# Optimization experiments

Measured on AMD Instinct MI355X. Metric: run time of the kernel, lower is better.

Reference implementation:

```python
import jax, jax.numpy as jnp
import numpy as np

B, D, E, T, H = 16384, 1024, 8, 4, 512


def setup_inputs() -> dict:
    key = jax.random.key(0)
    ks = jax.random.split(key, 7)
    s_e = 1.0 / np.sqrt(D)
    s_t = 1.0 / np.sqrt(H)
    return {
        "x": jax.random.normal(ks[0], (B, D), dtype=jnp.float32),
        "We": jax.random.uniform(ks[1], (E, D, H), minval=-s_e, maxval=s_e, dtype=jnp.float32),
        "be": jax.random.uniform(ks[2], (E, H), minval=-s_e, maxval=s_e, dtype=jnp.float32),
        "Wg": jax.random.uniform(ks[3], (T, D, E), minval=-s_e, maxval=s_e, dtype=jnp.float32),
        "bg": jax.random.uniform(ks[4], (T, E), minval=-s_e, maxval=s_e, dtype=jnp.float32),
        "Wt": jax.random.uniform(ks[5], (T, H, 1), minval=-s_t, maxval=s_t, dtype=jnp.float32),
        "bt": jax.random.uniform(ks[6], (T, 1), minval=-s_t, maxval=s_t, dtype=jnp.float32),
    }


def reference(x, We, be, Wg, bg, Wt, bt):
    # Experts: [B, E, H] -- batched GEMM over all experts at once
    expert_out = jnp.einsum("bd,edh->beh", x, We) + be[None, :, :]
    # Gates per task: logits [B, T, E], softmax over experts
    gate_logits = jnp.einsum("bd,tde->bte", x, Wg) + bg[None, :, :]
    gate_w = jax.nn.softmax(gate_logits, axis=-1)
    # Weighted sum of expert outputs per task: [B, T, H]
    mixed = jnp.einsum("bte,beh->bth", gate_w, expert_out)
    # Task heads: [B, T, 1]
    task_out = jnp.einsum("bth,tho->bto", mixed, Wt) + bt[None, :, :]
    # Match original: list of T tensors [B, 1] -> stacked [T, B, 1]
    return jnp.transpose(task_out, (1, 0, 2))
```

## Files before the change

### kernel.cpp

```cpp
#include <hip/hip_runtime.h>
#include <math.h>


typedef float  f32x4  __attribute__((ext_vector_type(4)));
typedef short  bf16x8 __attribute__((ext_vector_type(8)));

#define WFRAG_OFF_BYTES 262272
#define SCHED_FENCE() __builtin_amdgcn_sched_barrier(0)

__device__ __forceinline__ void cvt_pair(float f0, float f1, unsigned int& hi, unsigned int& lo) {
  unsigned int u0 = __float_as_uint(f0), u1 = __float_as_uint(f1);
  unsigned int r0 = u0 + 0x7FFFu + ((u0 >> 16) & 1u);
  unsigned int r1 = u1 + 0x7FFFu + ((u1 >> 16) & 1u);
  float h0 = __uint_as_float(r0 & 0xFFFF0000u);
  float h1 = __uint_as_float(r1 & 0xFFFF0000u);
  hi = (r0 >> 16) | (r1 & 0xFFFF0000u);
  float l0 = f0 - h0, l1 = f1 - h1;
  unsigned int s0 = __float_as_uint(l0), s1 = __float_as_uint(l1);
  unsigned int q0 = s0 + 0x7FFFu + ((s0 >> 16) & 1u);
  unsigned int q1 = s1 + 0x7FFFu + ((s1 >> 16) & 1u);
  lo = (q0 >> 16) | (q1 & 0xFFFF0000u);
}

__device__ __forceinline__ unsigned int cvtpk_bf16(float a, float b) {
  unsigned int r;
  asm("v_cvt_pk_bf16_f32 %0, %1, %2" : "=v"(r) : "v"(a), "v"(b));
  return r;
}
__device__ __forceinline__ void cvt_pair_fast(float f0, float f1, unsigned int& hi, unsigned int& lo) {
  unsigned int h = cvtpk_bf16(f0, f1);
  float h0 = __uint_as_float(h << 16);
  float h1 = __uint_as_float(h & 0xFFFF0000u);
  lo = cvtpk_bf16(f0 - h0, f1 - h1);
  hi = h;
}

__global__ __launch_bounds__(256) void mmoe_precompute(
    const float* __restrict__ We, const float* __restrict__ be,
    const float* __restrict__ Wg, const float* __restrict__ Wt,
    float* __restrict__ ws)
{
  float* Wcomb = ws;
  float* cbias = ws + 65536;
  const int tid = threadIdx.x, lane = tid & 63, w = tid >> 6;
  const int pairid = blockIdx.x * 4 + w;
  const int e = pairid >> 10, d = pairid & 1023;

  const float* werow = We + (size_t)pairid * 512;
  float a0 = 0.f, a1 = 0.f, a2 = 0.f, a3 = 0.f;
#pragma unroll
  for (int j = 0; j < 8; ++j) {
    int h = lane + j * 64;
    float wv = werow[h];
    a0 = fmaf(wv, Wt[h],        a0);
    a1 = fmaf(wv, Wt[512 + h],  a1);
    a2 = fmaf(wv, Wt[1024 + h], a2);
    a3 = fmaf(wv, Wt[1536 + h], a3);
  }
#pragma unroll
  for (int m = 1; m < 64; m <<= 1) {
    a0 += __shfl_xor(a0, m, 64); a1 += __shfl_xor(a1, m, 64);
    a2 += __shfl_xor(a2, m, 64); a3 += __shfl_xor(a3, m, 64);
  }
  if (lane == 0) {
    Wcomb[d * 64 + 32 + 0 * 8 + e] = a0;
    Wcomb[d * 64 + 32 + 1 * 8 + e] = a1;
    Wcomb[d * 64 + 32 + 2 * 8 + e] = a2;
    Wcomb[d * 64 + 32 + 3 * 8 + e] = a3;
  }
  if (e == 0 && lane < 32) {
    int t = lane >> 3, ee = lane & 7;
    Wcomb[d * 64 + t * 8 + ee] = Wg[t * 8192 + d * 8 + ee];
  }
  if (d == 0) {
    float b0 = 0.f, b1 = 0.f, b2 = 0.f, b3 = 0.f;
#pragma unroll
    for (int j = 0; j < 8; ++j) {
      int h = lane + j * 64;
      float bv = be[e * 512 + h];
      b0 = fmaf(bv, Wt[h],        b0);
      b1 = fmaf(bv, Wt[512 + h],  b1);
      b2 = fmaf(bv, Wt[1024 + h], b2);
      b3 = fmaf(bv, Wt[1536 + h], b3);
    }
#pragma unroll
    for (int m = 1; m < 64; m <<= 1) {
      b0 += __shfl_xor(b0, m, 64); b1 += __shfl_xor(b1, m, 64);
      b2 += __shfl_xor(b2, m, 64); b3 += __shfl_xor(b3, m, 64);
    }
    if (lane == 0) {
      cbias[0 * 8 + e] = b0; cbias[1 * 8 + e] = b1;
      cbias[2 * 8 + e] = b2; cbias[3 * 8 + e] = b3;
    }
  }
}

__global__ __launch_bounds__(256) void mmoe_swizzle(const float* __restrict__ Wc,
                                                    uint4* __restrict__ wf)
{
  const int idx = blockIdx.x * 256 + threadIdx.x;
  const int ks = idx >> 9;
  const int rem = idx & 511;
  const int vn = rem >> 6, l = rem & 63;
  const int v = vn >> 2, nf = vn & 3;
  const int n = nf * 16 + (l & 15);
  const int kbase = ks * 32 + (l >> 4) * 8;
  unsigned int pk[4];
#pragma unroll
  for (int p = 0; p < 4; ++p) {
    float f0 = Wc[(size_t)(kbase + 2 * p) * 64 + n];
    float f1 = Wc[(size_t)(kbase + 2 * p + 1) * 64 + n];
    unsigned int hi, lo;
    cvt_pair(f0, f1, hi, lo);
    pk[p] = v ? lo : hi;
  }
  uint4 val; val.x = pk[0]; val.y = pk[1]; val.z = pk[2]; val.w = pk[3];
  wf[idx] = val;
}

union UC { unsigned int u[4]; bf16x8 v; };

template <int S>
__device__ __forceinline__ void mmoe_step(
    const float4* __restrict__ xp0, const float4* __restrict__ xp1,
    const bf16x8* __restrict__ bptrw, int l,
    float4 (&xbuf)[4][2][2], bf16x8 (&breg)[2][8], f32x4 (&acc)[2][4])
{
  constexpr int D = S & 3;
  constexpr int P = S & 1;
  float4 xa0 = xbuf[D][0][0], xa1 = xbuf[D][0][1];
  float4 xb0 = xbuf[D][1][0], xb1 = xbuf[D][1][1];
  if constexpr (S + 4 < 8) {
    xbuf[D][0][0] = xp0[(S + 4) * 8];
    xbuf[D][0][1] = xp0[(S + 4) * 8 + 1];
    xbuf[D][1][0] = xp1[(S + 4) * 8];
    xbuf[D][1][1] = xp1[(S + 4) * 8 + 1];
  }
  UC A0h, A0l, A1h, A1l;
  cvt_pair_fast(xa0.x, xa0.y, A0h.u[0], A0l.u[0]);
  cvt_pair_fast(xa0.z, xa0.w, A0h.u[1], A0l.u[1]);
  cvt_pair_fast(xa1.x, xa1.y, A0h.u[2], A0l.u[2]);
  cvt_pair_fast(xa1.z, xa1.w, A0h.u[3], A0l.u[3]);
  cvt_pair_fast(xb0.x, xb0.y, A1h.u[0], A1l.u[0]);
  cvt_pair_fast(xb0.z, xb0.w, A1h.u[1], A1l.u[1]);
  cvt_pair_fast(xb1.x, xb1.y, A1h.u[2], A1l.u[2]);
  cvt_pair_fast(xb1.z, xb1.w, A1h.u[3], A1l.u[3]);

#pragma unroll
  for (int j = 0; j < 4; ++j)
    acc[0][j] = __builtin_amdgcn_mfma_f32_16x16x32_bf16(A0h.v, breg[P][j], acc[0][j], 0, 0, 0);
#pragma unroll
  for (int j = 0; j < 4; ++j)
    acc[1][j] = __builtin_amdgcn_mfma_f32_16x16x32_bf16(A1h.v, breg[P][j], acc[1][j], 0, 0, 0);
#pragma unroll
  for (int j = 0; j < 4; ++j)
    acc[0][j] = __builtin_amdgcn_mfma_f32_16x16x32_bf16(A0h.v, breg[P][j + 4], acc[0][j], 0, 0, 0);
#pragma unroll
  for (int j = 0; j < 4; ++j)
    acc[1][j] = __builtin_amdgcn_mfma_f32_16x16x32_bf16(A1h.v, breg[P][j + 4], acc[1][j], 0, 0, 0);
#pragma unroll
  for (int j = 0; j < 4; ++j)
    acc[0][j] = __builtin_amdgcn_mfma_f32_16x16x32_bf16(A0l.v, breg[P][j], acc[0][j], 0, 0, 0);
#pragma unroll
  for (int j = 0; j < 4; ++j)
    acc[1][j] = __builtin_amdgcn_mfma_f32_16x16x32_bf16(A1l.v, breg[P][j], acc[1][j], 0, 0, 0);
  if constexpr (S + 2 < 8) {
#pragma unroll
    for (int vn = 0; vn < 8; ++vn)
      breg[P][vn] = bptrw[(S + 2) * 512 + vn * 64 + l];
  }
  SCHED_FENCE();
}

__global__ __launch_bounds__(256, 2) void mmoe_main(
    const float* __restrict__ x,
    const float* __restrict__ bgp,
    const float* __restrict__ btp,
    const float* __restrict__ ws,
    float* __restrict__ out)
{
  __shared__ float cmat[4 * 2048];
  const int tid = threadIdx.x;
  const int l   = tid & 63;
  const int w   = tid >> 6;
  const int b0g = blockIdx.x * 32;
  const float* cbias = ws + 65536;
  const bf16x8* __restrict__ bptrw =
      (const bf16x8*)((const unsigned char*)ws + WFRAG_OFF_BYTES) + w * 8 * 512;

  const float4* __restrict__ xp0 =
      (const float4*)(x + (size_t)(b0g + (l & 15)) * 1024) + w * 64 + (l >> 4) * 2;
  const float4* __restrict__ xp1 = xp0 + 16 * 256;

  float4 xbuf[4][2][2];
  bf16x8 breg[2][8];
  f32x4  acc[2][4];
#pragma unroll
  for (int f = 0; f < 2; ++f)
#pragma unroll
    for (int nf = 0; nf < 4; ++nf) acc[f][nf] = (f32x4){0.f, 0.f, 0.f, 0.f};

#pragma unroll
  for (int p = 0; p < 4; ++p) {
    xbuf[p][0][0] = xp0[p * 8]; xbuf[p][0][1] = xp0[p * 8 + 1];
    xbuf[p][1][0] = xp1[p * 8]; xbuf[p][1][1] = xp1[p * 8 + 1];
  }
#pragma unroll
  for (int vn = 0; vn < 8; ++vn) breg[0][vn] = bptrw[vn * 64 + l];
#pragma unroll
  for (int vn = 0; vn < 8; ++vn) breg[1][vn] = bptrw[512 + vn * 64 + l];
  SCHED_FENCE();

  mmoe_step<0>(xp0, xp1, bptrw, l, xbuf, breg, acc);
  mmoe_step<1>(xp0, xp1, bptrw, l, xbuf, breg, acc);
  mmoe_step<2>(xp0, xp1, bptrw, l, xbuf, breg, acc);
  mmoe_step<3>(xp0, xp1, bptrw, l, xbuf, breg, acc);
  mmoe_step<4>(xp0, xp1, bptrw, l, xbuf, breg, acc);
  mmoe_step<5>(xp0, xp1, bptrw, l, xbuf, breg, acc);
  mmoe_step<6>(xp0, xp1, bptrw, l, xbuf, breg, acc);
  mmoe_step<7>(xp0, xp1, bptrw, l, xbuf, breg, acc);

#pragma unroll
  for (int f = 0; f < 2; ++f)
#pragma unroll
    for (int nf = 0; nf < 4; ++nf)
#pragma unroll
      for (int r = 0; r < 4; ++r)
        cmat[w * 2048 + (f * 16 + (l >> 4) * 4 + r) * 64 + nf * 16 + (l & 15)] = acc[f][nf][r];
  __syncthreads();

  if (tid < 128) {
    const int row = tid >> 2, t = tid & 3;
    float g[8] = {0.f, 0.f, 0.f, 0.f, 0.f, 0.f, 0.f, 0.f};
    float s[8] = {0.f, 0.f, 0.f, 0.f, 0.f, 0.f, 0.f, 0.f};
#pragma unroll
    for (int wv = 0; wv < 4; ++wv) {
      const float4 ga = *(const float4*)&cmat[wv * 2048 + row * 64 + t * 8];
      const float4 gb = *(const float4*)&cmat[wv * 2048 + row * 64 + t * 8 + 4];
      const float4 sa = *(const float4*)&cmat[wv * 2048 + row * 64 + 32 + t * 8];
      const float4 sb = *(const float4*)&cmat[wv * 2048 + row * 64 + 32 + t * 8 + 4];
      g[0] += ga.x; g[1] += ga.y; g[2] += ga.z; g[3] += ga.w;
      g[4] += gb.x; g[5] += gb.y; g[6] += gb.z; g[7] += gb.w;
      s[0] += sa.x; s[1] += sa.y; s[2] += sa.z; s[3] += sa.w;
      s[4] += sb.x; s[5] += sb.y; s[6] += sb.z; s[7] += sb.w;
    }
#pragma unroll
    for (int e = 0; e < 8; ++e) {
      g[e] += bgp[t * 8 + e];
      s[e] += cbias[t * 8 + e];
    }
    float m = g[0];
#pragma unroll
    for (int e = 1; e < 8; ++e) m = fmaxf(m, g[e]);
    float Z = 0.f, num = 0.f;
#pragma unroll
    for (int e = 0; e < 8; ++e) {
      float p2 = __expf(g[e] - m);
      Z += p2;
      num = fmaf(p2, s[e], num);
    }
    out[t * 16384 + b0g + row] = num / Z + btp[t];
  }
}

extern "C" void kernel_launch(void* const* d_in, const int* in_sizes, int n_in,
                              void* d_out, int out_size, void* d_ws, size_t ws_size,
                              hipStream_t stream) {
  const float* x  = (const float*)d_in[0];
  const float* We = (const float*)d_in[1];
  const float* be = (const float*)d_in[2];
  const float* Wg = (const float*)d_in[3];
  const float* bg = (const float*)d_in[4];
  const float* Wt = (const float*)d_in[5];
  const float* bt = (const float*)d_in[6];
  float* out = (float*)d_out;
  float* ws  = (float*)d_ws;

  uint4* wf = (uint4*)((unsigned char*)d_ws + WFRAG_OFF_BYTES);

  hipLaunchKernelGGL(mmoe_precompute, dim3(2048), dim3(256), 0, stream, We, be, Wg, Wt, ws);
  hipLaunchKernelGGL(mmoe_swizzle,    dim3(64),   dim3(256), 0, stream, ws, wf);
  hipLaunchKernelGGL(mmoe_main,       dim3(512),  dim3(256), 0, stream, x, bg, bt, ws, out);
}
```

Measured before the change: 122.8 us.

## Stage x tiles via direct global-to-LDS loads and split K across 8 waves

Replaces register-prefetched x loads with global_load_lds DMA into a swizzled double-buffered LDS staging area, synchronized with explicit vmcnt waits. Doubles the block to 512 threads so each of 8 waves handles a 128-wide K slice (4 steps instead of 8), with the cross-wave reduction summing 8 partials. The aim is to cut register pressure and improve latency hiding and occupancy. In exchange it adds LDS traffic, a larger shared footprint, and hand-tuned waitcnt counts that must match the issue order exactly.

After: 126.2 us. 1.03x slower.

```diff
diff --git a/kernel.cpp b/kernel.cpp
--- a/kernel.cpp
+++ b/kernel.cpp
@@ -7,6 +7,11 @@
 
 #define WFRAG_OFF_BYTES 262272
 #define SCHED_FENCE() __builtin_amdgcn_sched_barrier(0)
+
+__device__ __forceinline__ void lds_load16(const float* g, float* l) {
+  __builtin_amdgcn_global_load_lds((const __attribute__((address_space(1))) unsigned int*)g,
+                                   (__attribute__((address_space(3))) unsigned int*)l, 16, 0, 0);
+}
 
 __device__ __forceinline__ void cvt_pair(float f0, float f1, unsigned int& hi, unsigned int& lo) {
   unsigned int u0 = __float_as_uint(f0), u1 = __float_as_uint(f1);
@@ -122,20 +127,34 @@
 
 template <int S>
 __device__ __forceinline__ void mmoe_step(
-    const float4* __restrict__ xp0, const float4* __restrict__ xp1,
+    const float* __restrict__ xs0, const float* __restrict__ xs1,
+    const float* __restrict__ xs2, const float* __restrict__ xs3,
+    float* stage0, float* stage1,
+    int off00, int off01, int off10, int off11,
     const bf16x8* __restrict__ bptrw, int l,
-    float4 (&xbuf)[4][2][2], bf16x8 (&breg)[2][8], f32x4 (&acc)[2][4])
+    bf16x8 (&breg)[2][8], f32x4 (&acc)[2][4])
 {
-  constexpr int D = S & 3;
   constexpr int P = S & 1;
-  float4 xa0 = xbuf[D][0][0], xa1 = xbuf[D][0][1];
-  float4 xb0 = xbuf[D][1][0], xb1 = xbuf[D][1][1];
-  if constexpr (S + 4 < 8) {
-    xbuf[D][0][0] = xp0[(S + 4) * 8];
-    xbuf[D][0][1] = xp0[(S + 4) * 8 + 1];
-    xbuf[D][1][0] = xp1[(S + 4) * 8];
-    xbuf[D][1][1] = xp1[(S + 4) * 8 + 1];
-  }
+  if constexpr (S == 0) asm volatile("s_waitcnt vmcnt(20)" ::: "memory");
+  if constexpr (S == 1) asm volatile("s_waitcnt vmcnt(20)" ::: "memory");
+  if constexpr (S == 2) asm volatile("s_waitcnt vmcnt(20)" ::: "memory");
+  if constexpr (S == 3) asm volatile("s_waitcnt vmcnt(8)"  ::: "memory");
+  SCHED_FENCE();
+  const float* buf = P ? stage1 : stage0;
+  float4 xa0 = *(const float4*)(buf + off00);
+  float4 xa1 = *(const float4*)(buf + off01);
+  float4 xb0 = *(const float4*)(buf + off10);
+  float4 xb1 = *(const float4*)(buf + off11);
+  asm volatile("s_waitcnt lgkmcnt(0)" ::: "memory");
+  SCHED_FENCE();
+  if constexpr (S + 2 < 4) {
+    float* dst = P ? stage1 : stage0;
+    lds_load16(xs0 + (S + 2) * 32, dst + 0 * 256);
+    lds_load16(xs1 + (S + 2) * 32, dst + 1 * 256);
+    lds_load16(xs2 + (S + 2) * 32, dst + 2 * 256);
+    lds_load16(xs3 + (S + 2) * 32, dst + 3 * 256);
+  }
+  SCHED_FENCE();
   UC A0h, A0l, A1h, A1l;
   cvt_pair_fast(xa0.x, xa0.y, A0h.u[0], A0l.u[0]);
   cvt_pair_fast(xa0.z, xa0.w, A0h.u[1], A0l.u[1]);
@@ -145,7 +164,6 @@
   cvt_pair_fast(xb0.z, xb0.w, A1h.u[1], A1l.u[1]);
   cvt_pair_fast(xb1.x, xb1.y, A1h.u[2], A1l.u[2]);
   cvt_pair_fast(xb1.z, xb1.w, A1h.u[3], A1l.u[3]);
-
 #pragma unroll
   for (int j = 0; j < 4; ++j)
     acc[0][j] = __builtin_amdgcn_mfma_f32_16x16x32_bf16(A0h.v, breg[P][j], acc[0][j], 0, 0, 0);
@@ -164,7 +182,7 @@
 #pragma unroll
   for (int j = 0; j < 4; ++j)
     acc[1][j] = __builtin_amdgcn_mfma_f32_16x16x32_bf16(A1l.v, breg[P][j], acc[1][j], 0, 0, 0);
-  if constexpr (S + 2 < 8) {
+  if constexpr (S + 2 < 4) {
 #pragma unroll
     for (int vn = 0; vn < 8; ++vn)
       breg[P][vn] = bptrw[(S + 2) * 512 + vn * 64 + l];
@@ -172,27 +190,40 @@
   SCHED_FENCE();
 }
 
-__global__ __launch_bounds__(256, 2) void mmoe_main(
+__global__ __launch_bounds__(512, 4) void mmoe_main(
     const float* __restrict__ x,
     const float* __restrict__ bgp,
     const float* __restrict__ btp,
     const float* __restrict__ ws,
     float* __restrict__ out)
 {
-  __shared__ float cmat[4 * 2048];
+  __shared__ float smem[16384];
   const int tid = threadIdx.x;
   const int l   = tid & 63;
   const int w   = tid >> 6;
   const int b0g = blockIdx.x * 32;
   const float* cbias = ws + 65536;
   const bf16x8* __restrict__ bptrw =
-      (const bf16x8*)((const unsigned char*)ws + WFRAG_OFF_BYTES) + w * 8 * 512;
-
-  const float4* __restrict__ xp0 =
-      (const float4*)(x + (size_t)(b0g + (l & 15)) * 1024) + w * 64 + (l >> 4) * 2;
-  const float4* __restrict__ xp1 = xp0 + 16 * 256;
-
-  float4 xbuf[4][2][2];
+      (const bf16x8*)((const unsigned char*)ws + WFRAG_OFF_BYTES) + (size_t)w * 4 * 512;
+
+  float* stage0 = smem + w * 2048;
+  float* stage1 = smem + w * 2048 + 1024;
+
+  const int rsub = l >> 3;
+  const int csw  = (l & 7) ^ rsub;
+  const float* xs0 = x + (size_t)(b0g + 0 * 8 + rsub) * 1024 + w * 128 + csw * 4;
+  const float* xs1 = x + (size_t)(b0g + 1 * 8 + rsub) * 1024 + w * 128 + csw * 4;
+  const float* xs2 = x + (size_t)(b0g + 2 * 8 + rsub) * 1024 + w * 128 + csw * 4;
+  const float* xs3 = x + (size_t)(b0g + 3 * 8 + rsub) * 1024 + w * 128 + csw * 4;
+
+  const int o = l >> 4;
+  const int bx0 = ((o * 32 +  0) ^ ((l & 7) << 4)) >> 2;
+  const int bx1 = ((o * 32 + 16) ^ ((l & 7) << 4)) >> 2;
+  const int off00 = (l & 15) * 32 + bx0;
+  const int off01 = (l & 15) * 32 + bx1;
+  const int off10 = off00 + 512;
+  const int off11 = off01 + 512;
+
   bf16x8 breg[2][8];
   f32x4  acc[2][4];
 #pragma unroll
@@ -200,26 +231,27 @@
 #pragma unroll
     for (int nf = 0; nf < 4; ++nf) acc[f][nf] = (f32x4){0.f, 0.f, 0.f, 0.f};
 
-#pragma unroll
-  for (int p = 0; p < 4; ++p) {
-    xbuf[p][0][0] = xp0[p * 8]; xbuf[p][0][1] = xp0[p * 8 + 1];
-    xbuf[p][1][0] = xp1[p * 8]; xbuf[p][1][1] = xp1[p * 8 + 1];
-  }
+  lds_load16(xs0 + 0,  stage0 + 0 * 256);
+  lds_load16(xs1 + 0,  stage0 + 1 * 256);
+  lds_load16(xs2 + 0,  stage0 + 2 * 256);
+  lds_load16(xs3 + 0,  stage0 + 3 * 256);
+  lds_load16(xs0 + 32, stage1 + 0 * 256);
+  lds_load16(xs1 + 32, stage1 + 1 * 256);
+  lds_load16(xs2 + 32, stage1 + 2 * 256);
+  lds_load16(xs3 + 32, stage1 + 3 * 256);
+  SCHED_FENCE();
 #pragma unroll
   for (int vn = 0; vn < 8; ++vn) breg[0][vn] = bptrw[vn * 64 + l];
 #pragma unroll
   for (int vn = 0; vn < 8; ++vn) breg[1][vn] = bptrw[512 + vn * 64 + l];
   SCHED_FENCE();
 
-  mmoe_step<0>(xp0, xp1, bptrw, l, xbuf, breg, acc);
-  mmoe_step<1>(xp0, xp1, bptrw, l, xbuf, breg, acc);
-  mmoe_step<2>(xp0, xp1, bptrw, l, xbuf, breg, acc);
-  mmoe_step<3>(xp0, xp1, bptrw, l, xbuf, breg, acc);
-  mmoe_step<4>(xp0, xp1, bptrw, l, xbuf, breg, acc);
-  mmoe_step<5>(xp0, xp1, bptrw, l, xbuf, breg, acc);
-  mmoe_step<6>(xp0, xp1, bptrw, l, xbuf, breg, acc);
-  mmoe_step<7>(xp0, xp1, bptrw, l, xbuf, breg, acc);
-
+  mmoe_step<0>(xs0, xs1, xs2, xs3, stage0, stage1, off00, off01, off10, off11, bptrw, l, breg, acc);
+  mmoe_step<1>(xs0, xs1, xs2, xs3, stage0, stage1, off00, off01, off10, off11, bptrw, l, breg, acc);
+  mmoe_step<2>(xs0, xs1, xs2, xs3, stage0, stage1, off00, off01, off10, off11, bptrw, l, breg, acc);
+  mmoe_step<3>(xs0, xs1, xs2, xs3, stage0, stage1, off00, off01, off10, off11, bptrw, l, breg, acc);
+
+  float* cmat = smem;
 #pragma unroll
   for (int f = 0; f < 2; ++f)
 #pragma unroll
@@ -234,7 +266,7 @@
     float g[8] = {0.f, 0.f, 0.f, 0.f, 0.f, 0.f, 0.f, 0.f};
     float s[8] = {0.f, 0.f, 0.f, 0.f, 0.f, 0.f, 0.f, 0.f};
 #pragma unroll
-    for (int wv = 0; wv < 4; ++wv) {
+    for (int wv = 0; wv < 8; ++wv) {
       const float4 ga = *(const float4*)&cmat[wv * 2048 + row * 64 + t * 8];
       const float4 gb = *(const float4*)&cmat[wv * 2048 + row * 64 + t * 8 + 4];
       const float4 sa = *(const float4*)&cmat[wv * 2048 + row * 64 + 32 + t * 8];
@@ -280,5 +312,5 @@
 
   hipLaunchKernelGGL(mmoe_precompute, dim3(2048), dim3(256), 0, stream, We, be, Wg, Wt, ws);
   hipLaunchKernelGGL(mmoe_swizzle,    dim3(64),   dim3(256), 0, stream, ws, wf);
-  hipLaunchKernelGGL(mmoe_main,       dim3(512),  dim3(256), 0, stream, x, bg, bt, ws, out);
-}
+  hipLaunchKernelGGL(mmoe_main,       dim3(512),  dim3(512), 0, stream, x, bg, bt, ws, out);
+}
```
